# Performance work log

Measured on AMD Instinct MI355X. Metric: run time of the kernel, lower is better.

The kernel has to match this reference:

```python
import jax, jax.numpy as jnp
import numpy as np
from math import factorial, sqrt, pi

MUL = 8
LS = [0, 1, 2]                       # l values for both Rs_in and Rs_out
RS = [(MUL, l) for l in LS]
N_NODES = 20000
N_EDGES = 100000
FEAT = sum(m * (2 * l + 1) for m, l in RS)       # 72
R_TOT = sum(mo * mi * (2 * min(lo, li) + 1) for mo, lo in RS for mi, li in RS)  # 1216
L_MAX = max(LS) + max(LS)            # 4
RSH_DIM = (L_MAX + 1) ** 2           # 25
NB, H = 10, 100                      # radial basis size / hidden width
MIN_R, MAX_R = 0.7, 3.2
SWISH_SCALE = 1.679177               # e3nn rescaled swish factor


def _w3j_entry(j1, j2, j3, m1, m2, m3):
    # complex-basis Wigner 3j (Racah formula)
    if m1 + m2 + m3 != 0 or not (abs(j1 - j2) <= j3 <= j1 + j2):
        return 0.0
    t1, t2 = j2 - m1 - j3, j1 + m2 - j3
    kmin, kmax = max(0, t1, t2), min(j1 + j2 - j3, j1 - m1, j2 + m2)
    s = sum((-1) ** k / (factorial(k) * factorial(k - t1) * factorial(k - t2)
                         * factorial(j1 + j2 - j3 - k) * factorial(j1 - m1 - k) * factorial(j2 + m2 - k))
            for k in range(kmin, kmax + 1))
    pref = (-1) ** (j1 - j2 - m3) * sqrt(
        factorial(j1 + j2 - j3) * factorial(j1 - j2 + j3) * factorial(-j1 + j2 + j3) / factorial(j1 + j2 + j3 + 1)
        * factorial(j1 + m1) * factorial(j1 - m1) * factorial(j2 + m2) * factorial(j2 - m2)
        * factorial(j3 + m3) * factorial(j3 - m3))
    return pref * s


def _real_cob(l):
    # complex->real spherical-harmonic change of basis
    U = np.zeros((2 * l + 1, 2 * l + 1), dtype=complex)
    U[l, l] = 1.0
    s = 1.0 / np.sqrt(2.0)
    for m in range(1, l + 1):
        U[l + m, l + m] = (-1) ** m * s
        U[l + m, l - m] = s
        U[l - m, l - m] = 1j * s
        U[l - m, l + m] = -1j * ((-1) ** m) * s
    return U


def _wigner3j_real(l1, l2, l3):
    w = np.zeros((2 * l1 + 1, 2 * l2 + 1, 2 * l3 + 1))
    for m1 in range(-l1, l1 + 1):
        for m2 in range(-l2, l2 + 1):
            m3 = -m1 - m2
            if abs(m3) <= l3:
                w[m1 + l1, m2 + l2, m3 + l3] = _w3j_entry(l1, l2, l3, m1, m2, m3)
    T = np.einsum('am,bn,cp,mnp->abc', _real_cob(l1), _real_cob(l2), _real_cob(l3), w.astype(complex))
    C = T.real if np.linalg.norm(T.real) >= np.linalg.norm(T.imag) else T.imag
    n = np.linalg.norm(C)
    return (C / n if n > 0 else C).astype(np.float32)


# precomputed constants (coupling coefficients + normalization), as in MinimalNetwork.__init__
C3 = {(lo, li, lf): jnp.asarray(_wigner3j_real(lo, li, lf))
      for _, lo in RS for _, li in RS for lf in range(abs(lo - li), lo + li + 1)}


def _norm_coef():
    nc = np.zeros((len(RS), len(RS)), dtype=np.float32)
    for i, (_, lo) in enumerate(RS):
        num = sum(mi * (2 * min(lo, li) + 1) for mi, li in RS)
        nc[i, :] = sqrt(4 * pi) * sqrt(2 * lo + 1) / sqrt(num)
    return jnp.asarray(nc)

NORM = _norm_coef()


def _swish(x):
    return SWISH_SCALE * x * jax.nn.sigmoid(x)


def _radial(r, Ws):
    # GaussianRadialModel: gaussian basis -> 3 hidden swish layers -> linear out
    centers = jnp.linspace(MIN_R, MAX_R, NB)
    sigma = (MAX_R - MIN_R) / (NB - 1)
    x = jnp.exp(-(((r[:, None] - centers) / sigma) ** 2))
    for W in Ws[:-1]:
        x = _swish(x @ (W / jnp.sqrt(jnp.asarray(W.shape[0], x.dtype))))
    W = Ws[-1]
    return x @ (W / jnp.sqrt(jnp.asarray(W.shape[0], x.dtype)))


def _tensor_message(F_src, rsh, R):
    # F_src: [E, FEAT] gathered source features; rsh: [E, 25]; R: [E, R_TOT]
    E = F_src.shape[0]
    f_offs = np.cumsum([0] + [m * (2 * l + 1) for m, l in RS])
    msgs, r_off = [], 0
    for i, (U, lo) in enumerate(RS):
        acc = jnp.zeros((E, U, 2 * lo + 1), F_src.dtype)
        for j, (V, li) in enumerate(RS):
            nlf = 2 * min(lo, li) + 1
            Rb = R[:, r_off:r_off + U * V * nlf].reshape(E, U, V, nlf)
            r_off += U * V * nlf
            Fb = F_src[:, f_offs[j]:f_offs[j + 1]].reshape(E, V, 2 * li + 1)
            for fi, lf in enumerate(range(abs(lo - li), lo + li + 1)):
                # K[e,mo,mi] = sum_mf C3[mo,mi,mf] * Y_lf[e,mf]
                K = jnp.einsum('oif,ef->eoi', C3[(lo, li, lf)], rsh[:, lf * lf:(lf + 1) * (lf + 1)])
                acc = acc + NORM[i, j] * jnp.einsum('eoi,evi,euv->euo', K, Fb, Rb[..., fi])
        msgs.append(acc.reshape(E, -1))
    return jnp.concatenate(msgs, axis=-1)


def _forward(features, edge_index, radii, rsh, Ws):
    R = _radial(radii, Ws)                                     # [E, R_TOT]
    msg = _tensor_message(features[edge_index[0]], rsh, R)     # [E, FEAT]
    # scatter-add aggregation at target nodes (MessagePassing aggr='add')
    return jnp.zeros((features.shape[0], msg.shape[1]), msg.dtype).at[edge_index[1]].add(msg)


def setup_inputs() -> dict:
    key = jax.random.key(0)
    ks = jax.random.split(key, 8)
    features = jax.random.normal(ks[0], (N_NODES, FEAT), jnp.float32)
    edge_index = jax.random.randint(ks[1], (2, N_EDGES), 0, N_NODES)
    radii = MIN_R + (MAX_R - MIN_R) * jax.random.uniform(ks[2], (N_EDGES,), jnp.float32)
    rsh = jax.random.normal(ks[3], (N_EDGES, RSH_DIM), jnp.float32)
    W0 = jax.random.normal(ks[4], (NB, H), jnp.float32)
    W1 = jax.random.normal(ks[5], (H, H), jnp.float32)
    W2 = jax.random.normal(ks[6], (H, H), jnp.float32)
    W3 = jax.random.normal(ks[7], (H, R_TOT), jnp.float32)
    return {"features": features, "edge_index": edge_index, "radii": radii, "rsh": rsh,
            "W0": W0, "W1": W1, "W2": W2, "W3": W3}


def reference(features, edge_index, radii, rsh, W0, W1, W2, W3):
    return _forward(features, edge_index, radii, rsh, (W0, W1, W2, W3))
```

## Files before the change

kernel.cpp:

```cpp
#include <hip/hip_runtime.h>
#include <hip/hip_bf16.h>
#include <math.h>


#define FEATD 72
#define NCOL 1216
#define SWISH_SCALE 1.679177f

typedef __attribute__((ext_vector_type(8))) short bf16x8;
typedef __attribute__((ext_vector_type(4))) float f32x4;

constexpr int NCOMBO = 19;
constexpr int CB_LO[NCOMBO] = {0,0,0,1,1,1,1,1,1,1,2,2,2,2,2,2,2,2,2};
constexpr int CB_LI[NCOMBO] = {0,1,2,0,1,1,1,2,2,2,0,1,1,1,2,2,2,2,2};
constexpr int CB_LF[NCOMBO] = {0,1,2,1,0,1,2,1,2,3,2,1,2,3,0,1,2,3,4};
constexpr int CB_OFF[NCOMBO] = {0,1,10,35,44,53,80,125,170,245,350,375,420,495,600,625,700,825,1000};
constexpr int CB_SZ[NCOMBO]  = {1,9,25,9,9,27,45,45,75,105,25,45,75,105,25,75,125,175,225};
constexpr int C3TOT = 1225;

constexpr int C3OFFT[3][3][5] = {
  { {0,-1,-1,-1,-1}, {-1,1,-1,-1,-1}, {-1,-1,10,-1,-1} },
  { {-1,35,-1,-1,-1}, {44,53,80,-1,-1}, {-1,125,170,245,-1} },
  { {-1,-1,350,-1,-1}, {-1,375,420,495,-1}, {600,625,700,825,1000} }
};
constexpr int ROFFT[3][3] = {{0,64,128},{192,256,448},{640,704,896}};
constexpr int FOFFT[3]   = {0,8,32};

__device__ const double d_fact[11] = {1.,1.,2.,6.,24.,120.,720.,5040.,40320.,362880.,3628800.};

__device__ double w3j_entry(int j1,int j2,int j3,int m1,int m2,int m3){
  if (m1+m2+m3 != 0) return 0.0;
  int dj = j1-j2; if (dj<0) dj=-dj;
  if (j3 < dj || j3 > j1+j2) return 0.0;
  int t1 = j2 - m1 - j3, t2 = j1 + m2 - j3;
  int kmin = 0; if (t1>kmin) kmin=t1; if (t2>kmin) kmin=t2;
  int kmax = j1+j2-j3; if (j1-m1<kmax) kmax=j1-m1; if (j2+m2<kmax) kmax=j2+m2;
  double s = 0.0;
  for (int k=kmin;k<=kmax;++k){
    double den = d_fact[k]*d_fact[k-t1]*d_fact[k-t2]*d_fact[j1+j2-j3-k]
               * d_fact[j1-m1-k]*d_fact[j2+m2-k];
    s += ((k&1)? -1.0:1.0)/den;
  }
  double pref = sqrt(d_fact[j1+j2-j3]*d_fact[j1-j2+j3]*d_fact[-j1+j2+j3]/d_fact[j1+j2+j3+1]
               * d_fact[j1+m1]*d_fact[j1-m1]*d_fact[j2+m2]*d_fact[j2-m2]
               * d_fact[j3+m3]*d_fact[j3-m3]);
  int ex = j1-j2-m3;
  if (ex & 1) pref = -pref;
  return pref*s;
}

__device__ void cob(int l, int r, int c, double& re, double& im){
  re = 0.0; im = 0.0;
  int mr = r - l, mc = c - l;
  const double s = 0.70710678118654752440;
  if (mr == 0) { if (mc == 0) re = 1.0; return; }
  if (mr > 0) {
    if (mc == mr)       re = (mr & 1) ? -s : s;
    else if (mc == -mr) re = s;
  } else {
    int m = -mr;
    if (mc == -m)      im = s;
    else if (mc == m)  im = (m & 1) ? s : -s;
  }
}

__global__ void c3_build_kernel(double* __restrict__ Tre, double* __restrict__ Tim){
  int idx = blockIdx.x*64 + threadIdx.x;
  if (idx >= C3TOT) return;
  int c = 0;
  while (c+1 < NCOMBO && idx >= CB_OFF[c+1]) ++c;
  int lo = CB_LO[c], li = CB_LI[c], lf = CB_LF[c];
  int n2 = 2*li+1, n3 = 2*lf+1;
  int loc = idx - CB_OFF[c];
  int a = loc/(n2*n3), b = (loc/n3)%n2, g = loc%n3;
  double sre=0.0, sim=0.0;
  for (int m1=-lo; m1<=lo; ++m1){
    for (int m2=-li; m2<=li; ++m2){
      int m3 = -m1-m2;
      if (m3 < -lf || m3 > lf) continue;
      double w = w3j_entry(lo,li,lf,m1,m2,m3);
      if (w == 0.0) continue;
      double r1,i1,r2,i2,r3,i3;
      cob(lo, a, m1+lo, r1,i1);
      cob(li, b, m2+li, r2,i2);
      cob(lf, g, m3+lf, r3,i3);
      double rr = r1*r2 - i1*i2, ri = r1*i2 + i1*r2;
      double fr = rr*r3 - ri*i3, fi = rr*i3 + ri*r3;
      sre += fr*w; sim += fi*w;
    }
  }
  Tre[idx] = sre; Tim[idx] = sim;
}

__global__ void c3_norm_kernel(const double* __restrict__ Tre, const double* __restrict__ Tim,
                               float* __restrict__ C3f){
  int c = blockIdx.x;
  int off = CB_OFF[c], sz = CB_SZ[c];
  int t = threadIdx.x;
  double sre=0.0, sim=0.0;
  for (int p=t; p<sz; p+=64){ double x=Tre[off+p], y=Tim[off+p]; sre+=x*x; sim+=y*y; }
  for (int m=1; m<64; m<<=1){ sre += __shfl_xor(sre, m, 64); sim += __shfl_xor(sim, m, 64); }
  bool useRe = (sre >= sim);
  double n = sqrt(useRe ? sre : sim);
  double inv = (n > 0.0) ? 1.0/n : 1.0;
  for (int p=t; p<sz; p+=64){
    double v = useRe ? Tre[off+p] : Tim[off+p];
    C3f[off+p] = (float)(v*inv);
  }
}

__global__ __launch_bounds__(256) void prep_w3t_kernel(const float* __restrict__ W3,
                                                       __hip_bfloat16* __restrict__ W3t){
  int idx = blockIdx.x*256 + threadIdx.x;
  if (idx >= 1216*128) return;
  int cp = idx >> 7, k = idx & 127;
  int chunk = cp >> 6, r = cp & 63;
  int lo = CB_LO[chunk], li = CB_LI[chunk], lf = CB_LF[chunk];
  int lmin = lo<li ? lo : li;
  int nlf = 2*lmin+1;
  int fi = lf - (lo>li ? lo-li : li-lo);
  int c = ROFFT[lo][li] + r*nlf + fi;
  float v = (k < 100) ? 0.1f*W3[(size_t)k*NCOL + c] : 0.f;
  int swz = (r*16 + (k>>3)) ^ (r&7);
  W3t[(size_t)chunk*8192 + swz*8 + (k&7)] = __float2bfloat16(v);
}

__global__ __launch_bounds__(256) void prep_wt_kernel(const float* __restrict__ W1,
                                                      const float* __restrict__ W2,
                                                      __hip_bfloat16* __restrict__ W1t,
                                                      __hip_bfloat16* __restrict__ W2t){
  int idx = blockIdx.x*256 + threadIdx.x;
  constexpr int HALF = 112*128;
  if (idx >= 2*HALF) return;
  const float* W = (idx < HALF) ? W1 : W2;
  __hip_bfloat16* Wt = (idx < HALF) ? W1t : W2t;
  int r = (idx < HALF) ? idx : idx - HALF;
  int o = r >> 7, k = r & 127;
  float v = (o < 100 && k < 100) ? 0.1f*W[k*100+o] : 0.f;
  int swz = (o*16 + (k>>3)) ^ (o&7);
  Wt[swz*8 + (k&7)] = __float2bfloat16(v);
}

__device__ __forceinline__ float swishf(float s){
  return SWISH_SCALE * s / (1.f + __expf(-s));
}

__device__ __forceinline__ void stage_w(const __hip_bfloat16* __restrict__ Wt,
                                        char* sW, int t)
{
  const int lane = t & 63, wv = t >> 6;
  const char* g = (const char*)Wt;
  #pragma unroll
  for (int i=0; i<7; ++i){
    const char* gsrc = g + (i*256 + wv*64 + lane)*16;
    __builtin_amdgcn_global_load_lds(
        (const __attribute__((address_space(1))) unsigned int*)gsrc,
        (__attribute__((address_space(3))) unsigned int*)(sW + i*4096 + wv*1024),
        16, 0, 0);
  }
}

__device__ __forceinline__ void radial_layer_lds(
    const __hip_bfloat16* __restrict__ sIn,
    const char* __restrict__ sW,
    __hip_bfloat16* __restrict__ sOut,
    int wv, int lr, int lq)
{
  bf16x8 bf[4];
  #pragma unroll
  for (int ks=0; ks<4; ++ks)
    bf[ks] = *(const bf16x8*)&sIn[(wv*16+lr)*136 + ks*32 + lq*8];
  f32x4 acc[7] = {};
  #pragma unroll
  for (int ks=0; ks<4; ++ks)
    #pragma unroll
    for (int ot=0; ot<7; ++ot){
      const int row = ot*16 + lr;
      const int u = (row*16 + ks*4 + lq) ^ (row & 7);
      bf16x8 a = *(const bf16x8*)(sW + u*16);
      acc[ot] = __builtin_amdgcn_mfma_f32_16x16x32_bf16(a, bf[ks], acc[ot], 0, 0, 0);
    }
  #pragma unroll
  for (int ot=0; ot<7; ++ot){
    __hip_bfloat16 hv[4];
    #pragma unroll
    for (int r=0; r<4; ++r)
      hv[r] = __float2bfloat16(swishf(acc[ot][r]));
    *(short4*)&sOut[(wv*16+lr)*136 + ot*16 + lq*4] = *(short4*)hv;
  }
  {
    int lane = lq*16 + lr;
    int row = lane & 15, q = lane >> 4;
    short4 z = {0,0,0,0};
    *(short4*)&sOut[(wv*16+row)*136 + 112 + q*4] = z;
  }
}

__global__ __launch_bounds__(256,2) void radial_mfma_kernel(
    const float* __restrict__ radii, const float* __restrict__ W0,
    const __hip_bfloat16* __restrict__ W1t, const __hip_bfloat16* __restrict__ W2t,
    __hip_bfloat16* __restrict__ h_bf, int E)
{
  __shared__ float sbas[640];
  __shared__ __align__(16) __hip_bfloat16 sA[64*136];
  __shared__ __align__(16) __hip_bfloat16 sB[64*136];
  __shared__ __align__(16) char sW[28672];
  const int t = threadIdx.x;
  const int et0 = blockIdx.x*64;

  stage_w(W1t, sW, t);

  for (int p=t; p<640; p+=256){
    int er = p/10, k = p%10;
    int eg = et0 + er;
    float r = (eg < E) ? radii[eg] : 0.f;
    float c = 0.7f + (2.5f/9.0f)*(float)k;
    float d = (r - c) * (9.0f/2.5f);
    sbas[p] = __expf(-d*d);
  }
  __syncthreads();
  for (int p=t; p<6400; p+=256){
    int er = p/100, o = p%100;
    float s = 0.f;
    #pragma unroll
    for (int k=0;k<10;++k) s += sbas[er*10+k]*W0[k*100+o];
    sA[er*136+o] = __float2bfloat16(swishf(s*0.3162277660168379f));
  }
  for (int p=t; p<64*36; p+=256){
    int er = p/36, k = 100 + p%36;
    sA[er*136+k] = __float2bfloat16(0.f);
  }
  __syncthreads();

  const int lane = t & 63, wv = t >> 6;
  const int lr = lane & 15, lq = lane >> 4;

  radial_layer_lds(sA, sW, sB, wv, lr, lq);
  __syncthreads();
  stage_w(W2t, sW, t);
  __syncthreads();
  radial_layer_lds(sB, sW, sA, wv, lr, lq);
  __builtin_amdgcn_wave_barrier();
  {
    const float4* sm = (const float4*)(sA + (size_t)(wv*16)*136);
    float4* gm = (float4*)(h_bf + (size_t)(et0 + wv*16)*136);
    for (int p=lane; p<272; p+=64) gm[p] = sm[p];
  }
}

__global__ __launch_bounds__(256) void hist_kernel(const int* __restrict__ ei,
                                                   int* __restrict__ deg, int E){
  int e = blockIdx.x*256 + threadIdx.x;
  if (e < E) atomicAdd(&deg[ei[E+e]], 1);
}

__global__ __launch_bounds__(256) void scan_kernel(const int* __restrict__ deg,
                                                   int* __restrict__ off,
                                                   int* __restrict__ cursor, int N, int E){
  __shared__ int part[256], spref[256];
  const int t = threadIdx.x;
  const int CH = (N + 255)/256;
  int lo = t*CH, hi = lo+CH < N ? lo+CH : N;
  int s = 0;
  for (int n=lo; n<hi; ++n) s += deg[n];
  part[t] = s;
  __syncthreads();
  if (t == 0){
    int run = 0;
    for (int i=0;i<256;++i){ spref[i] = run; run += part[i]; }
  }
  __syncthreads();
  int run = spref[t];
  for (int n=lo; n<hi; ++n){ off[n] = run; cursor[n] = run; run += deg[n]; }
  if (t == 255) off[N] = E;
}

__global__ __launch_bounds__(256) void fill_kernel(const int* __restrict__ ei,
                                                   int* __restrict__ cursor,
                                                   int* __restrict__ eid, int E){
  int e = blockIdx.x*256 + threadIdx.x;
  if (e < E){
    int idx = atomicAdd(&cursor[ei[E+e]], 1);
    eid[idx] = e;
  }
}

__global__ __launch_bounds__(64) void gather_kernel(const float* __restrict__ msg,
                                                    const int* __restrict__ off,
                                                    const int* __restrict__ eid,
                                                    float* __restrict__ out, int N){
  const int n = blockIdx.x;
  const int t = threadIdx.x;
  const int s = off[n], e1 = off[n+1];
  float a0 = 0.f, a1 = 0.f;
  for (int i=s; i<e1; ++i){
    const float* m = msg + (size_t)eid[i]*FEATD;
    a0 += m[t];
    if (t < 8) a1 += m[64+t];
  }
  out[(size_t)n*FEATD + t] = a0;
  if (t < 8) out[(size_t)n*FEATD + 64 + t] = a1;
}

constexpr int OF_W   = 0;
constexpr int OF_RT  = 16384;
constexpr int OF_ACC = 33792;
constexpr int OF_F   = 44032;
constexpr int OF_KV  = 63488;
constexpr int OF_C3  = 76288;
constexpr int OF_SRC = 81188;
constexpr int SMEM_SZ = 81444;

__device__ __forceinline__ void stage_chunk(const __hip_bfloat16* __restrict__ W3t,
                                            int chunk, char* sW, int t)
{
  const int lane = t & 63, wv = t >> 6;
  const char* g = (const char*)W3t + (size_t)chunk*16384;
  #pragma unroll
  for (int r=0; r<4; ++r){
    const char* gsrc = g + (wv*256 + r*64 + lane)*16;
    __builtin_amdgcn_global_load_lds(
        (const __attribute__((address_space(1))) unsigned int*)gsrc,
        (__attribute__((address_space(3))) unsigned int*)(sW + wv*4096 + r*1024),
        16, 0, 0);
  }
}

template<int LO,int LI,int LF>
__device__ __forceinline__ void kv_sec(float* kvb, const float* sC3,
                                       const float* __restrict__ rshrow,
                                       int e, int role)
{
  constexpr int NO = 2*LO+1, NI = 2*LI+1, NF = 2*LF+1;
  constexpr int C3B = C3OFFT[LO][LI][LF];
  float y[NF];
  #pragma unroll
  for (int mf=0; mf<NF; ++mf) y[mf] = rshrow[LF*LF + mf];
  for (int it = role; it < NO*NI; it += 4){
    float s = 0.f;
    #pragma unroll
    for (int mf=0; mf<NF; ++mf) s += sC3[C3B + it*NF + mf] * y[mf];
    kvb[e*25 + it] = s;
  }
}

template<int LO,int LI>
__device__ __forceinline__ void consume_sec(
    const float* sRt, const float* sFf, const float* kvb, float* sAcc,
    int e, int role)
{
  constexpr int NO = 2*LO+1, NI = 2*LI+1;
  constexpr int FO = FOFFT[LI];
  float H[2][NI];
  #pragma unroll
  for (int du=0; du<2; ++du)
    #pragma unroll
    for (int mi=0; mi<NI; ++mi) H[du][mi] = 0.f;

  #pragma unroll
  for (int vg=0; vg<2; ++vg){
    float fb[4*NI];
    #pragma unroll
    for (int p=0; p<NI; ++p)
      *(f32x4*)&fb[p*4] = *(const f32x4*)&sFf[e*76 + FO + vg*4*NI + p*4];
    #pragma unroll
    for (int du=0; du<2; ++du){
      const int u = role*2 + du;
      f32x4 rv = *(const f32x4*)&sRt[e*68 + u*8 + vg*4];
      #pragma unroll
      for (int v=0; v<4; ++v)
        #pragma unroll
        for (int mi=0; mi<NI; ++mi)
          H[du][mi] += rv[v] * fb[v*NI + mi];
    }
  }
  const int u0 = role*2, u1 = role*2 + 1;
  const int b0 = e*40 + ((LO==0) ? u0 : (LO==1) ? u0*3 : u0*5);
  const int b1 = e*40 + ((LO==0) ? u1 : (LO==1) ? u1*3 : u1*5);
  #pragma unroll
  for (int o=0; o<NO; ++o){
    float s0 = 0.f, s1 = 0.f;
    #pragma unroll
    for (int mi=0; mi<NI; ++mi){
      float kvv = kvb[e*25 + o*NI + mi];
      s0 += kvv * H[0][mi];
      s1 += kvv * H[1][mi];
    }
    sAcc[b0 + o] += s0;
    sAcc[b1 + o] += s1;
  }
}

__device__ __forceinline__ void mfma_sec(const char* sW, float* sRt,
                                         const bf16x8 (&hf)[4],
                                         int wv, int lr, int lq)
{
  f32x4 a4[4] = {};
  #pragma unroll
  for (int ks=0; ks<4; ++ks){
    #pragma unroll
    for (int ct=0; ct<4; ++ct){
      const int row = ct*16 + lr;
      const int u   = (row*16 + (ks*4 + lq)) ^ (row & 7);
      bf16x8 a = *(const bf16x8*)(sW + u*16);
      a4[ct] = __builtin_amdgcn_mfma_f32_16x16x32_bf16(a, hf[ks], a4[ct], 0, 0, 0);
    }
  }
  #pragma unroll
  for (int ct=0; ct<4; ++ct)
    *(f32x4*)&sRt[(wv*16 + lr)*68 + ct*16 + lq*4] = a4[ct];
}

template<int J0,int W>
__device__ __forceinline__ void flush_group(float* sAcc, float* __restrict__ msg,
                                            int eb, int t, float nrm)
{
  const int lane = t & 63, wv = t >> 6;
  __builtin_amdgcn_wave_barrier();
  for (int p = lane; p < 16*W; p += 64){
    int el = wv*16 + p/W, j = p%W;
    msg[(size_t)(eb + el)*FEATD + J0 + j] = nrm * sAcc[el*40 + j];
    sAcc[el*40 + j] = 0.f;
  }
  __builtin_amdgcn_wave_barrier();
}

template<int LO,int LI,int LF,int PLO,int PLI,int PFLUSH,int CUR>
__device__ __forceinline__ void phase_pl(
    int chunk, const __hip_bfloat16* __restrict__ W3t, const bf16x8 (&hf)[4],
    char* sW, float* sRt, float* sFf, float* sKV, const float* sC3,
    const float* __restrict__ rshrow, float* sAcc,
    float* __restrict__ msg, int eb, int t)
{
  const int e = t >> 2, role = t & 3;
  const int lane = t & 63, wv = t >> 6;
  const int lr = lane & 15, lq = lane >> 4;

  __syncthreads();
  stage_chunk(W3t, chunk, sW, t);

  kv_sec<LO,LI,LF>(sKV + CUR*1600, sC3, rshrow, e, role);
  if constexpr (PLO >= 0)
    consume_sec<PLO,PLI>(sRt, sFf, sKV + (1-CUR)*1600, sAcc, e, role);
  if constexpr (PFLUSH == 0)
    flush_group<0,8>(sAcc, msg, eb, t, 0.72360125f);
  if constexpr (PFLUSH == 1)
    flush_group<8,24>(sAcc, msg, eb, t, 0.8204867f);

  __syncthreads();
  mfma_sec(sW, sRt, hf, wv, lr, lq);
  __builtin_amdgcn_wave_barrier();
}

__global__ __launch_bounds__(256,2) void fused_kernel(
    const float* __restrict__ feats, const int* __restrict__ ei,
    const float* __restrict__ rsh, const __hip_bfloat16* __restrict__ h_bf,
    const __hip_bfloat16* __restrict__ W3t, const float* __restrict__ C3g,
    float* __restrict__ msg, int E)
{
  __shared__ __align__(16) char smem[SMEM_SZ];
  char*  sW   = smem + OF_W;
  float* sRt  = (float*)(smem + OF_RT);
  float* sAcc = (float*)(smem + OF_ACC);
  float* sFf  = (float*)(smem + OF_F);
  float* sKV  = (float*)(smem + OF_KV);
  float* sC3  = (float*)(smem + OF_C3);
  int*   sSrc = (int*)(smem + OF_SRC);

  const int t = threadIdx.x;
  const int eb = blockIdx.x*64;

  bf16x8 hf[4];
  {
    const int lane = t & 63, wv = t >> 6;
    const int lr = lane & 15, lq = lane >> 4;
    const __hip_bfloat16* hrow = h_bf + (size_t)(eb + wv*16 + lr)*136;
    #pragma unroll
    for (int ks=0; ks<4; ++ks)
      hf[ks] = *(const bf16x8*)&hrow[ks*32 + lq*8];
  }
  for (int p=t; p<2560; p+=256) sAcc[p] = 0.f;
  for (int p=t; p<64; p+=256){
    int e = eb + p;
    sSrc[p] = (e < E) ? ei[e] : 0;
  }
  for (int p=t; p<C3TOT; p+=256) sC3[p] = C3g[p];
  __syncthreads();
  for (int p=t; p<64*72; p+=256){
    int el = p/72, j = p%72;
    sFf[el*76 + j] = feats[(size_t)sSrc[el]*72 + j];
  }
  __syncthreads();

  int eg = eb + (t >> 2); if (eg > E-1) eg = E-1;
  const float* rshrow = rsh + (size_t)eg*25;

  phase_pl<0,0,0, -1,-1, -1, 0>( 0, W3t, hf, sW, sRt, sFf, sKV, sC3, rshrow, sAcc, msg, eb, t);
  phase_pl<0,1,1,  0, 0, -1, 1>( 1, W3t, hf, sW, sRt, sFf, sKV, sC3, rshrow, sAcc, msg, eb, t);
  phase_pl<0,2,2,  0, 1, -1, 0>( 2, W3t, hf, sW, sRt, sFf, sKV, sC3, rshrow, sAcc, msg, eb, t);
  phase_pl<1,0,1,  0, 2,  0, 1>( 3, W3t, hf, sW, sRt, sFf, sKV, sC3, rshrow, sAcc, msg, eb, t);
  phase_pl<1,1,0,  1, 0, -1, 0>( 4, W3t, hf, sW, sRt, sFf, sKV, sC3, rshrow, sAcc, msg, eb, t);
  phase_pl<1,1,1,  1, 1, -1, 1>( 5, W3t, hf, sW, sRt, sFf, sKV, sC3, rshrow, sAcc, msg, eb, t);
  phase_pl<1,1,2,  1, 1, -1, 0>( 6, W3t, hf, sW, sRt, sFf, sKV, sC3, rshrow, sAcc, msg, eb, t);
  phase_pl<1,2,1,  1, 1, -1, 1>( 7, W3t, hf, sW, sRt, sFf, sKV, sC3, rshrow, sAcc, msg, eb, t);
  phase_pl<1,2,2,  1, 2, -1, 0>( 8, W3t, hf, sW, sRt, sFf, sKV, sC3, rshrow, sAcc, msg, eb, t);
  phase_pl<1,2,3,  1, 2, -1, 1>( 9, W3t, hf, sW, sRt, sFf, sKV, sC3, rshrow, sAcc, msg, eb, t);
  phase_pl<2,0,2,  1, 2,  1, 0>(10, W3t, hf, sW, sRt, sFf, sKV, sC3, rshrow, sAcc, msg, eb, t);
  phase_pl<2,1,1,  2, 0, -1, 1>(11, W3t, hf, sW, sRt, sFf, sKV, sC3, rshrow, sAcc, msg, eb, t);
  phase_pl<2,1,2,  2, 1, -1, 0>(12, W3t, hf, sW, sRt, sFf, sKV, sC3, rshrow, sAcc, msg, eb, t);
  phase_pl<2,1,3,  2, 1, -1, 1>(13, W3t, hf, sW, sRt, sFf, sKV, sC3, rshrow, sAcc, msg, eb, t);
  phase_pl<2,2,0,  2, 1, -1, 0>(14, W3t, hf, sW, sRt, sFf, sKV, sC3, rshrow, sAcc, msg, eb, t);
  phase_pl<2,2,1,  2, 2, -1, 1>(15, W3t, hf, sW, sRt, sFf, sKV, sC3, rshrow, sAcc, msg, eb, t);
  phase_pl<2,2,2,  2, 2, -1, 0>(16, W3t, hf, sW, sRt, sFf, sKV, sC3, rshrow, sAcc, msg, eb, t);
  phase_pl<2,2,3,  2, 2, -1, 1>(17, W3t, hf, sW, sRt, sFf, sKV, sC3, rshrow, sAcc, msg, eb, t);
  phase_pl<2,2,4,  2, 2, -1, 0>(18, W3t, hf, sW, sRt, sFf, sKV, sC3, rshrow, sAcc, msg, eb, t);

  {
    const int e = t >> 2, role = t & 3;
    consume_sec<2,2>(sRt, sFf, sKV + 0*1600, sAcc, e, role);
    flush_group<32,40>(sAcc, msg, eb, t, 0.9341652f);
  }
}

extern "C" void kernel_launch(void* const* d_in, const int* in_sizes, int n_in,
                              void* d_out, int out_size, void* d_ws, size_t ws_size,
                              hipStream_t stream)
{
  const float* feats = (const float*)d_in[0];
  const int*   ei    = (const int*)d_in[1];
  const float* radii = (const float*)d_in[2];
  const float* rsh   = (const float*)d_in[3];
  const float* W0    = (const float*)d_in[4];
  const float* W1    = (const float*)d_in[5];
  const float* W2    = (const float*)d_in[6];
  const float* W3    = (const float*)d_in[7];
  float* out = (float*)d_out;
  const int E = in_sizes[2];
  const int N = in_sizes[0]/FEATD;

  const int EPAD = ((E + 63)/64)*64;
  const int NBLK = EPAD/64;

  char* ws = (char*)d_ws;
  size_t off_b = 0;
  float*  C3f = (float*)(ws + off_b);  off_b += 8192;
  double* Tre = (double*)(ws + off_b); off_b += 12288;
  double* Tim = (double*)(ws + off_b); off_b += 12288;
  __hip_bfloat16* W3t = (__hip_bfloat16*)(ws + off_b); off_b += 335872;
  __hip_bfloat16* W1t = (__hip_bfloat16*)(ws + off_b); off_b += 30720;
  __hip_bfloat16* W2t = (__hip_bfloat16*)(ws + off_b); off_b += 30720;
  __hip_bfloat16* h_bf = (__hip_bfloat16*)(ws + off_b); off_b += (size_t)EPAD*272;
  float* msg = (float*)(ws + off_b);   off_b += (size_t)EPAD*FEATD*4;
  int* deg    = (int*)(ws + off_b);    off_b += (size_t)N*4;
  int* offv   = (int*)(ws + off_b);    off_b += (size_t)(N+1)*4;
  int* cursor = (int*)(ws + off_b);    off_b += (size_t)N*4;
  int* eid    = (int*)(ws + off_b);    off_b += (size_t)E*4;

  c3_build_kernel<<<dim3((C3TOT+63)/64), dim3(64), 0, stream>>>(Tre, Tim);
  c3_norm_kernel<<<dim3(NCOMBO), dim3(64), 0, stream>>>(Tre, Tim, C3f);
  prep_w3t_kernel<<<dim3((1216*128+255)/256), dim3(256), 0, stream>>>(W3, W3t);
  prep_wt_kernel<<<dim3((2*112*128+255)/256), dim3(256), 0, stream>>>(W1, W2, W1t, W2t);

  hipMemsetAsync(deg, 0, (size_t)N*4, stream);
  hist_kernel<<<dim3((E+255)/256), dim3(256), 0, stream>>>(ei, deg, E);
  scan_kernel<<<dim3(1), dim3(256), 0, stream>>>(deg, offv, cursor, N, E);
  fill_kernel<<<dim3((E+255)/256), dim3(256), 0, stream>>>(ei, cursor, eid, E);

  radial_mfma_kernel<<<dim3(NBLK), dim3(256), 0, stream>>>(radii, W0, W1t, W2t, h_bf, E);
  fused_kernel<<<dim3(NBLK), dim3(256), 0, stream>>>(feats, ei, rsh, h_bf, W3t, C3f, msg, E);
  gather_kernel<<<dim3(N), dim3(64), 0, stream>>>(msg, offv, eid, out, N);
}
```

Before: 374.5 us.

## Fuse radial MLP into tensor-product kernel and merge setup kernels

Moves the radial MLP (basis expansion plus two bf16 MFMA layers) into the start of the fused message kernel. The hidden activations now stay in shared memory instead of going through a global h_bf buffer. The two C3 Clebsch-Gordan build/normalize kernels are merged into one per-combo kernel, and the three weight-prep kernels into one, which cuts launch count. The cost is a fused kernel with a longer serial prologue and reused shared-memory regions, which may lower overlap or occupancy.

```diff
diff --git a/kernel.cpp b/kernel.cpp
--- a/kernel.cpp
+++ b/kernel.cpp
@@ -64,187 +64,75 @@
   }
 }
 
-__global__ void c3_build_kernel(double* __restrict__ Tre, double* __restrict__ Tim){
-  int idx = blockIdx.x*64 + threadIdx.x;
-  if (idx >= C3TOT) return;
-  int c = 0;
-  while (c+1 < NCOMBO && idx >= CB_OFF[c+1]) ++c;
-  int lo = CB_LO[c], li = CB_LI[c], lf = CB_LF[c];
-  int n2 = 2*li+1, n3 = 2*lf+1;
-  int loc = idx - CB_OFF[c];
-  int a = loc/(n2*n3), b = (loc/n3)%n2, g = loc%n3;
-  double sre=0.0, sim=0.0;
-  for (int m1=-lo; m1<=lo; ++m1){
-    for (int m2=-li; m2<=li; ++m2){
-      int m3 = -m1-m2;
-      if (m3 < -lf || m3 > lf) continue;
-      double w = w3j_entry(lo,li,lf,m1,m2,m3);
-      if (w == 0.0) continue;
-      double r1,i1,r2,i2,r3,i3;
-      cob(lo, a, m1+lo, r1,i1);
-      cob(li, b, m2+li, r2,i2);
-      cob(lf, g, m3+lf, r3,i3);
-      double rr = r1*r2 - i1*i2, ri = r1*i2 + i1*r2;
-      double fr = rr*r3 - ri*i3, fi = rr*i3 + ri*r3;
-      sre += fr*w; sim += fi*w;
+__global__ void c3_combined_kernel(float* __restrict__ C3f){
+  __shared__ double sre[225], sim[225];
+  const int c = blockIdx.x;
+  const int lo = CB_LO[c], li = CB_LI[c], lf = CB_LF[c];
+  const int off = CB_OFF[c], sz = CB_SZ[c];
+  const int n2 = 2*li+1, n3 = 2*lf+1;
+  const int t = threadIdx.x;
+
+  for (int p=t; p<sz; p+=64){
+    int a = p/(n2*n3), b = (p/n3)%n2, g = p%n3;
+    double re=0.0, im=0.0;
+    for (int m1=-lo; m1<=lo; ++m1){
+      for (int m2=-li; m2<=li; ++m2){
+        int m3 = -m1-m2;
+        if (m3 < -lf || m3 > lf) continue;
+        double w = w3j_entry(lo,li,lf,m1,m2,m3);
+        if (w == 0.0) continue;
+        double r1,i1,r2,i2,r3,i3;
+        cob(lo, a, m1+lo, r1,i1);
+        cob(li, b, m2+li, r2,i2);
+        cob(lf, g, m3+lf, r3,i3);
+        double rr = r1*r2 - i1*i2, ri = r1*i2 + i1*r2;
+        double fr = rr*r3 - ri*i3, fi = rr*i3 + ri*r3;
+        re += fr*w; im += fi*w;
+      }
     }
-  }
-  Tre[idx] = sre; Tim[idx] = sim;
-}
-
-__global__ void c3_norm_kernel(const double* __restrict__ Tre, const double* __restrict__ Tim,
-                               float* __restrict__ C3f){
-  int c = blockIdx.x;
-  int off = CB_OFF[c], sz = CB_SZ[c];
-  int t = threadIdx.x;
-  double sre=0.0, sim=0.0;
-  for (int p=t; p<sz; p+=64){ double x=Tre[off+p], y=Tim[off+p]; sre+=x*x; sim+=y*y; }
-  for (int m=1; m<64; m<<=1){ sre += __shfl_xor(sre, m, 64); sim += __shfl_xor(sim, m, 64); }
-  bool useRe = (sre >= sim);
-  double n = sqrt(useRe ? sre : sim);
+    sre[p] = re; sim[p] = im;
+  }
+  __syncthreads();
+  double s2r=0.0, s2i=0.0;
+  for (int p=t; p<sz; p+=64){ double x=sre[p], y=sim[p]; s2r+=x*x; s2i+=y*y; }
+  for (int m=1; m<64; m<<=1){ s2r += __shfl_xor(s2r, m, 64); s2i += __shfl_xor(s2i, m, 64); }
+  bool useRe = (s2r >= s2i);
+  double n = sqrt(useRe ? s2r : s2i);
   double inv = (n > 0.0) ? 1.0/n : 1.0;
   for (int p=t; p<sz; p+=64){
-    double v = useRe ? Tre[off+p] : Tim[off+p];
+    double v = useRe ? sre[p] : sim[p];
     C3f[off+p] = (float)(v*inv);
   }
 }
 
-__global__ __launch_bounds__(256) void prep_w3t_kernel(const float* __restrict__ W3,
-                                                       __hip_bfloat16* __restrict__ W3t){
+__global__ __launch_bounds__(256) void prep_combined_kernel(
+    const float* __restrict__ W3, const float* __restrict__ W1,
+    const float* __restrict__ W2, __hip_bfloat16* __restrict__ W3t,
+    __hip_bfloat16* __restrict__ W1t, __hip_bfloat16* __restrict__ W2t)
+{
   int idx = blockIdx.x*256 + threadIdx.x;
-  if (idx >= 1216*128) return;
-  int cp = idx >> 7, k = idx & 127;
-  int chunk = cp >> 6, r = cp & 63;
-  int lo = CB_LO[chunk], li = CB_LI[chunk], lf = CB_LF[chunk];
-  int lmin = lo<li ? lo : li;
-  int nlf = 2*lmin+1;
-  int fi = lf - (lo>li ? lo-li : li-lo);
-  int c = ROFFT[lo][li] + r*nlf + fi;
-  float v = (k < 100) ? 0.1f*W3[(size_t)k*NCOL + c] : 0.f;
-  int swz = (r*16 + (k>>3)) ^ (r&7);
-  W3t[(size_t)chunk*8192 + swz*8 + (k&7)] = __float2bfloat16(v);
-}
-
-__global__ __launch_bounds__(256) void prep_wt_kernel(const float* __restrict__ W1,
-                                                      const float* __restrict__ W2,
-                                                      __hip_bfloat16* __restrict__ W1t,
-                                                      __hip_bfloat16* __restrict__ W2t){
-  int idx = blockIdx.x*256 + threadIdx.x;
+  constexpr int NW3 = 1216*128;
   constexpr int HALF = 112*128;
-  if (idx >= 2*HALF) return;
-  const float* W = (idx < HALF) ? W1 : W2;
-  __hip_bfloat16* Wt = (idx < HALF) ? W1t : W2t;
-  int r = (idx < HALF) ? idx : idx - HALF;
-  int o = r >> 7, k = r & 127;
-  float v = (o < 100 && k < 100) ? 0.1f*W[k*100+o] : 0.f;
-  int swz = (o*16 + (k>>3)) ^ (o&7);
-  Wt[swz*8 + (k&7)] = __float2bfloat16(v);
-}
-
-__device__ __forceinline__ float swishf(float s){
-  return SWISH_SCALE * s / (1.f + __expf(-s));
-}
-
-__device__ __forceinline__ void stage_w(const __hip_bfloat16* __restrict__ Wt,
-                                        char* sW, int t)
-{
-  const int lane = t & 63, wv = t >> 6;
-  const char* g = (const char*)Wt;
-  #pragma unroll
-  for (int i=0; i<7; ++i){
-    const char* gsrc = g + (i*256 + wv*64 + lane)*16;
-    __builtin_amdgcn_global_load_lds(
-        (const __attribute__((address_space(1))) unsigned int*)gsrc,
-        (__attribute__((address_space(3))) unsigned int*)(sW + i*4096 + wv*1024),
-        16, 0, 0);
-  }
-}
-
-__device__ __forceinline__ void radial_layer_lds(
-    const __hip_bfloat16* __restrict__ sIn,
-    const char* __restrict__ sW,
-    __hip_bfloat16* __restrict__ sOut,
-    int wv, int lr, int lq)
-{
-  bf16x8 bf[4];
-  #pragma unroll
-  for (int ks=0; ks<4; ++ks)
-    bf[ks] = *(const bf16x8*)&sIn[(wv*16+lr)*136 + ks*32 + lq*8];
-  f32x4 acc[7] = {};
-  #pragma unroll
-  for (int ks=0; ks<4; ++ks)
-    #pragma unroll
-    for (int ot=0; ot<7; ++ot){
-      const int row = ot*16 + lr;
-      const int u = (row*16 + ks*4 + lq) ^ (row & 7);
-      bf16x8 a = *(const bf16x8*)(sW + u*16);
-      acc[ot] = __builtin_amdgcn_mfma_f32_16x16x32_bf16(a, bf[ks], acc[ot], 0, 0, 0);
-    }
-  #pragma unroll
-  for (int ot=0; ot<7; ++ot){
-    __hip_bfloat16 hv[4];
-    #pragma unroll
-    for (int r=0; r<4; ++r)
-      hv[r] = __float2bfloat16(swishf(acc[ot][r]));
-    *(short4*)&sOut[(wv*16+lr)*136 + ot*16 + lq*4] = *(short4*)hv;
-  }
-  {
-    int lane = lq*16 + lr;
-    int row = lane & 15, q = lane >> 4;
-    short4 z = {0,0,0,0};
-    *(short4*)&sOut[(wv*16+row)*136 + 112 + q*4] = z;
-  }
-}
-
-__global__ __launch_bounds__(256,2) void radial_mfma_kernel(
-    const float* __restrict__ radii, const float* __restrict__ W0,
-    const __hip_bfloat16* __restrict__ W1t, const __hip_bfloat16* __restrict__ W2t,
-    __hip_bfloat16* __restrict__ h_bf, int E)
-{
-  __shared__ float sbas[640];
-  __shared__ __align__(16) __hip_bfloat16 sA[64*136];
-  __shared__ __align__(16) __hip_bfloat16 sB[64*136];
-  __shared__ __align__(16) char sW[28672];
-  const int t = threadIdx.x;
-  const int et0 = blockIdx.x*64;
-
-  stage_w(W1t, sW, t);
-
-  for (int p=t; p<640; p+=256){
-    int er = p/10, k = p%10;
-    int eg = et0 + er;
-    float r = (eg < E) ? radii[eg] : 0.f;
-    float c = 0.7f + (2.5f/9.0f)*(float)k;
-    float d = (r - c) * (9.0f/2.5f);
-    sbas[p] = __expf(-d*d);
-  }
-  __syncthreads();
-  for (int p=t; p<6400; p+=256){
-    int er = p/100, o = p%100;
-    float s = 0.f;
-    #pragma unroll
-    for (int k=0;k<10;++k) s += sbas[er*10+k]*W0[k*100+o];
-    sA[er*136+o] = __float2bfloat16(swishf(s*0.3162277660168379f));
-  }
-  for (int p=t; p<64*36; p+=256){
-    int er = p/36, k = 100 + p%36;
-    sA[er*136+k] = __float2bfloat16(0.f);
-  }
-  __syncthreads();
-
-  const int lane = t & 63, wv = t >> 6;
-  const int lr = lane & 15, lq = lane >> 4;
-
-  radial_layer_lds(sA, sW, sB, wv, lr, lq);
-  __syncthreads();
-  stage_w(W2t, sW, t);
-  __syncthreads();
-  radial_layer_lds(sB, sW, sA, wv, lr, lq);
-  __builtin_amdgcn_wave_barrier();
-  {
-    const float4* sm = (const float4*)(sA + (size_t)(wv*16)*136);
-    float4* gm = (float4*)(h_bf + (size_t)(et0 + wv*16)*136);
-    for (int p=lane; p<272; p+=64) gm[p] = sm[p];
+  if (idx < NW3){
+    int cp = idx >> 7, k = idx & 127;
+    int chunk = cp >> 6, r = cp & 63;
+    int lo = CB_LO[chunk], li = CB_LI[chunk], lf = CB_LF[chunk];
+    int lmin = lo<li ? lo : li;
+    int nlf = 2*lmin+1;
+    int fi = lf - (lo>li ? lo-li : li-lo);
+    int c = ROFFT[lo][li] + r*nlf + fi;
+    float v = (k < 100) ? 0.1f*W3[(size_t)k*NCOL + c] : 0.f;
+    int swz = (r*16 + (k>>3)) ^ (r&7);
+    W3t[(size_t)chunk*8192 + swz*8 + (k&7)] = __float2bfloat16(v);
+  } else if (idx < NW3 + 2*HALF){
+    int r2 = idx - NW3;
+    const float* W = (r2 < HALF) ? W1 : W2;
+    __hip_bfloat16* Wt = (r2 < HALF) ? W1t : W2t;
+    int r = (r2 < HALF) ? r2 : r2 - HALF;
+    int o = r >> 7, k = r & 127;
+    float v = (o < 100 && k < 100) ? 0.1f*W[k*100+o] : 0.f;
+    int swz = (o*16 + (k>>3)) ^ (o&7);
+    Wt[swz*8 + (k&7)] = __float2bfloat16(v);
   }
 }
 
@@ -311,6 +199,66 @@
 constexpr int OF_SRC = 81188;
 constexpr int SMEM_SZ = 81444;
 
+constexpr int OF_RW   = 0;
+constexpr int OF_BAS  = 28672;
+constexpr int OF_HA   = 31232;
+constexpr int OF_HB   = 48640;
+
+__device__ __forceinline__ float swishf(float s){
+  return SWISH_SCALE * s / (1.f + __expf(-s));
+}
+
+__device__ __forceinline__ void stage_w(const __hip_bfloat16* __restrict__ Wt,
+                                        char* sW, int t)
+{
+  const int lane = t & 63, wv = t >> 6;
+  const char* g = (const char*)Wt;
+  #pragma unroll
+  for (int i=0; i<7; ++i){
+    const char* gsrc = g + (i*256 + wv*64 + lane)*16;
+    __builtin_amdgcn_global_load_lds(
+        (const __attribute__((address_space(1))) unsigned int*)gsrc,
+        (__attribute__((address_space(3))) unsigned int*)(sW + i*4096 + wv*1024),
+        16, 0, 0);
+  }
+}
+
+__device__ __forceinline__ void radial_layer_lds(
+    const __hip_bfloat16* __restrict__ sIn,
+    const char* __restrict__ sW,
+    __hip_bfloat16* __restrict__ sOut,
+    int wv, int lr, int lq)
+{
+  bf16x8 bf[4];
+  #pragma unroll
+  for (int ks=0; ks<4; ++ks)
+    bf[ks] = *(const bf16x8*)&sIn[(wv*16+lr)*136 + ks*32 + lq*8];
+  f32x4 acc[7] = {};
+  #pragma unroll
+  for (int ks=0; ks<4; ++ks)
+    #pragma unroll
+    for (int ot=0; ot<7; ++ot){
+      const int row = ot*16 + lr;
+      const int u = (row*16 + ks*4 + lq) ^ (row & 7);
+      bf16x8 a = *(const bf16x8*)(sW + u*16);
+      acc[ot] = __builtin_amdgcn_mfma_f32_16x16x32_bf16(a, bf[ks], acc[ot], 0, 0, 0);
+    }
+  #pragma unroll
+  for (int ot=0; ot<7; ++ot){
+    __hip_bfloat16 hv[4];
+    #pragma unroll
+    for (int r=0; r<4; ++r)
+      hv[r] = __float2bfloat16(swishf(acc[ot][r]));
+    *(short4*)&sOut[(wv*16+lr)*136 + ot*16 + lq*4] = *(short4*)hv;
+  }
+  {
+    int lane = lq*16 + lr;
+    int row = lane & 15, q = lane >> 4;
+    short4 z = {0,0,0,0};
+    *(short4*)&sOut[(wv*16+row)*136 + 112 + q*4] = z;
+  }
+}
+
 __device__ __forceinline__ void stage_chunk(const __hip_bfloat16* __restrict__ W3t,
                                             int chunk, char* sW, int t)
 {
@@ -454,7 +402,9 @@
 
 __global__ __launch_bounds__(256,2) void fused_kernel(
     const float* __restrict__ feats, const int* __restrict__ ei,
-    const float* __restrict__ rsh, const __hip_bfloat16* __restrict__ h_bf,
+    const float* __restrict__ radii, const float* __restrict__ rsh,
+    const float* __restrict__ W0,
+    const __hip_bfloat16* __restrict__ W1t, const __hip_bfloat16* __restrict__ W2t,
     const __hip_bfloat16* __restrict__ W3t, const float* __restrict__ C3g,
     float* __restrict__ msg, int E)
 {
@@ -466,19 +416,54 @@
   float* sKV  = (float*)(smem + OF_KV);
   float* sC3  = (float*)(smem + OF_C3);
   int*   sSrc = (int*)(smem + OF_SRC);
+  char*  sWr  = smem + OF_RW;
+  float* sbas = (float*)(smem + OF_BAS);
+  __hip_bfloat16* hA = (__hip_bfloat16*)(smem + OF_HA);
+  __hip_bfloat16* hB = (__hip_bfloat16*)(smem + OF_HB);
 
   const int t = threadIdx.x;
   const int eb = blockIdx.x*64;
+  const int lane = t & 63, wv = t >> 6;
+  const int lr = lane & 15, lq = lane >> 4;
+
+  stage_w(W1t, sWr, t);
+
+  for (int p=t; p<640; p+=256){
+    int er = p/10, k = p%10;
+    int eg = eb + er;
+    float r = (eg < E) ? radii[eg] : 0.f;
+    float c = 0.7f + (2.5f/9.0f)*(float)k;
+    float d = (r - c) * (9.0f/2.5f);
+    sbas[p] = __expf(-d*d);
+  }
+  __syncthreads();
+  for (int p=t; p<6400; p+=256){
+    int er = p/100, o = p%100;
+    float s = 0.f;
+    #pragma unroll
+    for (int k=0;k<10;++k) s += sbas[er*10+k]*W0[k*100+o];
+    hA[er*136+o] = __float2bfloat16(swishf(s*0.3162277660168379f));
+  }
+  for (int p=t; p<64*36; p+=256){
+    int er = p/36, k = 100 + p%36;
+    hA[er*136+k] = __float2bfloat16(0.f);
+  }
+  __syncthreads();
+
+  radial_layer_lds(hA, sWr, hB, wv, lr, lq);
+  __syncthreads();
+  stage_w(W2t, sWr, t);
+  __syncthreads();
+  radial_layer_lds(hB, sWr, hA, wv, lr, lq);
+  __builtin_amdgcn_wave_barrier();
 
   bf16x8 hf[4];
-  {
-    const int lane = t & 63, wv = t >> 6;
-    const int lr = lane & 15, lq = lane >> 4;
-    const __hip_bfloat16* hrow = h_bf + (size_t)(eb + wv*16 + lr)*136;
-    #pragma unroll
-    for (int ks=0; ks<4; ++ks)
-      hf[ks] = *(const bf16x8*)&hrow[ks*32 + lq*8];
-  }
+  #pragma unroll
+  for (int ks=0; ks<4; ++ks)
+    hf[ks] = *(const bf16x8*)&hA[(wv*16+lr)*136 + ks*32 + lq*8];
+
+  __syncthreads();
+
   for (int p=t; p<2560; p+=256) sAcc[p] = 0.f;
   for (int p=t; p<64; p+=256){
     int e = eb + p;
@@ -544,29 +529,25 @@
   char* ws = (char*)d_ws;
   size_t off_b = 0;
   float*  C3f = (float*)(ws + off_b);  off_b += 8192;
-  double* Tre = (double*)(ws + off_b); off_b += 12288;
-  double* Tim = (double*)(ws + off_b); off_b += 12288;
   __hip_bfloat16* W3t = (__hip_bfloat16*)(ws + off_b); off_b += 335872;
   __hip_bfloat16* W1t = (__hip_bfloat16*)(ws + off_b); off_b += 30720;
   __hip_bfloat16* W2t = (__hip_bfloat16*)(ws + off_b); off_b += 30720;
-  __hip_bfloat16* h_bf = (__hip_bfloat16*)(ws + off_b); off_b += (size_t)EPAD*272;
   float* msg = (float*)(ws + off_b);   off_b += (size_t)EPAD*FEATD*4;
   int* deg    = (int*)(ws + off_b);    off_b += (size_t)N*4;
   int* offv   = (int*)(ws + off_b);    off_b += (size_t)(N+1)*4;
   int* cursor = (int*)(ws + off_b);    off_b += (size_t)N*4;
   int* eid    = (int*)(ws + off_b);    off_b += (size_t)E*4;
 
-  c3_build_kernel<<<dim3((C3TOT+63)/64), dim3(64), 0, stream>>>(Tre, Tim);
-  c3_norm_kernel<<<dim3(NCOMBO), dim3(64), 0, stream>>>(Tre, Tim, C3f);
-  prep_w3t_kernel<<<dim3((1216*128+255)/256), dim3(256), 0, stream>>>(W3, W3t);
-  prep_wt_kernel<<<dim3((2*112*128+255)/256), dim3(256), 0, stream>>>(W1, W2, W1t, W2t);
+  c3_combined_kernel<<<dim3(NCOMBO), dim3(64), 0, stream>>>(C3f);
+  prep_combined_kernel<<<dim3((1216*128 + 2*112*128 + 255)/256), dim3(256), 0, stream>>>(
+      W3, W1, W2, W3t, W1t, W2t);
 
   hipMemsetAsync(deg, 0, (size_t)N*4, stream);
   hist_kernel<<<dim3((E+255)/256), dim3(256), 0, stream>>>(ei, deg, E);
   scan_kernel<<<dim3(1), dim3(256), 0, stream>>>(deg, offv, cursor, N, E);
   fill_kernel<<<dim3((E+255)/256), dim3(256), 0, stream>>>(ei, cursor, eid, E);
 
-  radial_mfma_kernel<<<dim3(NBLK), dim3(256), 0, stream>>>(radii, W0, W1t, W2t, h_bf, E);
-  fused_kernel<<<dim3(NBLK), dim3(256), 0, stream>>>(feats, ei, rsh, h_bf, W3t, C3f, msg, E);
+  fused_kernel<<<dim3(NBLK), dim3(256), 0, stream>>>(
+      feats, ei, radii, rsh, W0, W1t, W2t, W3t, C3f, msg, E);
   gather_kernel<<<dim3(N), dim3(64), 0, stream>>>(msg, offv, eid, out, N);
 }
```

New measurement: 405.3 us. +8.2%, slower.
